# Performance work log

Measured on AMD Instinct MI355X. Metric: run time of the kernel, lower is better.

The kernel has to match this reference:

```python
import jax, jax.numpy as jnp
import numpy as np

TOPK = 2
NUM_EXPERTS = 8


def setup_inputs() -> dict:
    key = jax.random.key(0)
    k1, k2 = jax.random.split(key)
    T, H, E = 16384, 2048, NUM_EXPERTS
    x = jax.random.normal(k1, (T, H), dtype=jnp.float32)
    W = jax.random.normal(k2, (E, H), dtype=jnp.float32) * (1.0 / np.sqrt(H))
    return {"x": x, "W": W}


def reference(x, W):
    # gating: [T, H] @ [H, E] -> [T, E]
    logits = jnp.einsum("th,eh->te", x, W)
    # top-k expert selection (largest, sorted desc, matching torch.topk)
    top_logits, top_indices = jax.lax.top_k(logits, TOPK)
    # softmax over the k selected logits, computed in fp32 (torch: dtype=float32 then type_as)
    scores = jax.nn.softmax(top_logits.astype(jnp.float32), axis=-1).astype(logits.dtype)
    # histogram of expert assignments (torch.histc -> float counts)
    tokens_per_expert = jnp.bincount(top_indices.reshape(-1), length=NUM_EXPERTS).astype(jnp.float32)
    return scores, top_indices, tokens_per_expert
```

## Files before the change

kernel.cpp:

```cpp
#include <hip/hip_runtime.h>
#include <math.h>

#define HDIM 2048
#define NEXP 8
#define TB 4
#define BLOCK 256
#define WAVES_PB 4
#define TOK_PB (WAVES_PB * TB)
#define CH 256
#define NCH (HDIM / CH)

__global__ __launch_bounds__(BLOCK, 4) void
router_main(const float* __restrict__ x,
            const float* __restrict__ W,
            float* __restrict__ out_scores,
            float* __restrict__ out_idx,
            float* __restrict__ hist,
            int T)
{
    __shared__ float4 xs[2][WAVES_PB][TB][64];
    __shared__ int cnt[NEXP];
    if (threadIdx.x < NEXP) cnt[threadIdx.x] = 0;
    __syncthreads();

    const int lane = threadIdx.x & 63;
    const int wv   = threadIdx.x >> 6;
    const int tok0 = blockIdx.x * TOK_PB + wv * TB;

    const float* xsrc[TB];
#pragma unroll
    for (int t = 0; t < TB; ++t) {
        int tt = tok0 + t; if (tt > T - 1) tt = T - 1;
        xsrc[t] = x + (size_t)tt * HDIM + lane * 4;
    }
    const float* wb = W + lane * 4;

    float acc[TB * NEXP];
#pragma unroll
    for (int i = 0; i < TB * NEXP; ++i) acc[i] = 0.f;

#pragma unroll
    for (int t = 0; t < TB; ++t)
        __builtin_amdgcn_global_load_lds(
            (const __attribute__((address_space(1))) void*)(xsrc[t]),
            (__attribute__((address_space(3))) void*)&xs[0][wv][t][0],
            16, 0, 0);

#pragma unroll 1
    for (int c = 0; c < NCH; ++c) {
        const int h = c * CH;

        float4 w[NEXP];
#pragma unroll
        for (int e = 0; e < NEXP; ++e)
            w[e] = *reinterpret_cast<const float4*>(wb + (size_t)e * HDIM + h);

        asm volatile("" ::: "memory");

        if (c + 1 < NCH) {
#pragma unroll
            for (int t = 0; t < TB; ++t)
                __builtin_amdgcn_global_load_lds(
                    (const __attribute__((address_space(1))) void*)(xsrc[t] + h + CH),
                    (__attribute__((address_space(3))) void*)&xs[(c + 1) & 1][wv][t][0],
                    16, 0, 0);
        }

        asm volatile("s_waitcnt vmcnt(8)" ::: "memory");

#pragma unroll
        for (int t = 0; t < TB; ++t) {
            const float4 xv = xs[c & 1][wv][t][lane];
#pragma unroll
            for (int e = 0; e < NEXP; ++e) {
                float a = acc[t * NEXP + e];
                a = fmaf(xv.x, w[e].x, a);
                a = fmaf(xv.y, w[e].y, a);
                a = fmaf(xv.z, w[e].z, a);
                a = fmaf(xv.w, w[e].w, a);
                acc[t * NEXP + e] = a;
            }
        }
    }

#pragma unroll
    for (int j = 0; j < 32; ++j) acc[j] += __shfl_xor(acc[j], 32, 64);

#define FOLD(SM)                                                          \
    {                                                                     \
        const bool up = (lane & SM) != 0;                                 \
        _Pragma("unroll")                                                 \
        for (int j = 0; j < SM; ++j) {                                    \
            float keep = up ? acc[j + SM] : acc[j];                       \
            float send = up ? acc[j] : acc[j + SM];                       \
            acc[j] = keep + __shfl_xor(send, SM, 64);                     \
        }                                                                 \
    }
    FOLD(16) FOLD(8) FOLD(4) FOLD(2) FOLD(1)
#undef FOLD

    const int e_my  = lane & 7;
    const int t_loc = (lane & 31) >> 3;
    const float mylg = acc[0];

    float v1 = mylg;
    int   i1 = e_my;
#pragma unroll
    for (int m = 1; m <= 4; m <<= 1) {
        float ov = __shfl_xor(v1, m, 64);
        int   oi = __shfl_xor(i1, m, 64);
        if (ov > v1 || (ov == v1 && oi < i1)) { v1 = ov; i1 = oi; }
    }
    float v2 = (e_my == i1) ? -3.402823466e+38f : mylg;
    int   i2 = e_my;
#pragma unroll
    for (int m = 1; m <= 4; m <<= 1) {
        float ov = __shfl_xor(v2, m, 64);
        int   oi = __shfl_xor(i2, m, 64);
        if (ov > v2 || (ov == v2 && oi < i2)) { v2 = ov; i2 = oi; }
    }

    const float ed  = expf(v2 - v1);
    const float inv = 1.0f / (1.0f + ed);

    const int tok = tok0 + t_loc;
    if (lane < 32 && e_my == 0 && tok < T) {
        *reinterpret_cast<float2*>(out_scores + 2 * tok) = make_float2(inv, ed * inv);
        *reinterpret_cast<float2*>(out_idx    + 2 * tok) = make_float2((float)i1, (float)i2);
        atomicAdd(&cnt[i1], 1);
        atomicAdd(&cnt[i2], 1);
    }

    __syncthreads();
    if (threadIdx.x < NEXP)
        atomicAdd(&hist[threadIdx.x], (float)cnt[threadIdx.x]);
}

extern "C" void kernel_launch(void* const* d_in, const int* in_sizes, int n_in,
                              void* d_out, int out_size, void* d_ws, size_t ws_size,
                              hipStream_t stream)
{
    const float* x = (const float*)d_in[0];
    const float* W = (const float*)d_in[1];
    const int T = in_sizes[0] / HDIM;

    float* out        = (float*)d_out;
    float* out_scores = out;
    float* out_idx    = out + (size_t)2 * T;
    float* hist       = out + (size_t)4 * T;

    hipMemsetAsync(hist, 0, NEXP * sizeof(float), stream);

    const int nblocks = (T + TOK_PB - 1) / TOK_PB;
    router_main<<<nblocks, BLOCK, 0, stream>>>(x, W, out_scores, out_idx, hist, T);
}
```

Measured before the change: 39.96 us.

## Stage full gate weights in LDS, load x directly into registers

Result: slower. 42.37 us (+6.0%).

```diff
diff --git a/kernel.cpp b/kernel.cpp
--- a/kernel.cpp
+++ b/kernel.cpp
@@ -4,8 +4,8 @@
 #define HDIM 2048
 #define NEXP 8
 #define TB 4
-#define BLOCK 256
-#define WAVES_PB 4
+#define BLOCK 512
+#define WAVES_PB 8
 #define TOK_PB (WAVES_PB * TB)
 #define CH 256
 #define NCH (HDIM / CH)
@@ -18,8 +18,16 @@
             float* __restrict__ hist,
             int T)
 {
-    __shared__ float4 xs[2][WAVES_PB][TB][64];
+    __shared__ float wlds[NEXP][HDIM];
     __shared__ int cnt[NEXP];
+
+    {
+        const float4* __restrict__ Wv = reinterpret_cast<const float4*>(W);
+        float4* wl = reinterpret_cast<float4*>(&wlds[0][0]);
+#pragma unroll
+        for (int j = 0; j < (NEXP * HDIM / 4) / BLOCK; ++j)
+            wl[threadIdx.x + j * BLOCK] = Wv[threadIdx.x + j * BLOCK];
+    }
     if (threadIdx.x < NEXP) cnt[threadIdx.x] = 0;
     __syncthreads();
 
@@ -27,58 +35,50 @@
     const int wv   = threadIdx.x >> 6;
     const int tok0 = blockIdx.x * TOK_PB + wv * TB;
 
-    const float* xsrc[TB];
+    const float* xb[TB];
 #pragma unroll
     for (int t = 0; t < TB; ++t) {
         int tt = tok0 + t; if (tt > T - 1) tt = T - 1;
-        xsrc[t] = x + (size_t)tt * HDIM + lane * 4;
+        xb[t] = x + (size_t)tt * HDIM + lane * 4;
     }
-    const float* wb = W + lane * 4;
 
     float acc[TB * NEXP];
 #pragma unroll
     for (int i = 0; i < TB * NEXP; ++i) acc[i] = 0.f;
 
 #pragma unroll
-    for (int t = 0; t < TB; ++t)
-        __builtin_amdgcn_global_load_lds(
-            (const __attribute__((address_space(1))) void*)(xsrc[t]),
-            (__attribute__((address_space(3))) void*)&xs[0][wv][t][0],
-            16, 0, 0);
-
-#pragma unroll 1
     for (int c = 0; c < NCH; ++c) {
-        const int h = c * CH;
-
-        float4 w[NEXP];
+        const int h = c * CH + lane * 4;
+        float4 xv[TB];
 #pragma unroll
-        for (int e = 0; e < NEXP; ++e)
-            w[e] = *reinterpret_cast<const float4*>(wb + (size_t)e * HDIM + h);
-
-        asm volatile("" ::: "memory");
-
-        if (c + 1 < NCH) {
-#pragma unroll
-            for (int t = 0; t < TB; ++t)
-                __builtin_amdgcn_global_load_lds(
-                    (const __attribute__((address_space(1))) void*)(xsrc[t] + h + CH),
-                    (__attribute__((address_space(3))) void*)&xs[(c + 1) & 1][wv][t][0],
-                    16, 0, 0);
-        }
-
-        asm volatile("s_waitcnt vmcnt(8)" ::: "memory");
+        for (int t = 0; t < TB; ++t)
+            xv[t] = *reinterpret_cast<const float4*>(xb[t] + c * CH);
 
 #pragma unroll
-        for (int t = 0; t < TB; ++t) {
-            const float4 xv = xs[c & 1][wv][t][lane];
+        for (int half = 0; half < 2; ++half) {
+            const int b = half * 4;
+            float4 w0 = *reinterpret_cast<const float4*>(&wlds[b + 0][h]);
+            float4 w1 = *reinterpret_cast<const float4*>(&wlds[b + 1][h]);
+            float4 w2 = *reinterpret_cast<const float4*>(&wlds[b + 2][h]);
+            float4 w3 = *reinterpret_cast<const float4*>(&wlds[b + 3][h]);
 #pragma unroll
-            for (int e = 0; e < NEXP; ++e) {
-                float a = acc[t * NEXP + e];
-                a = fmaf(xv.x, w[e].x, a);
-                a = fmaf(xv.y, w[e].y, a);
-                a = fmaf(xv.z, w[e].z, a);
-                a = fmaf(xv.w, w[e].w, a);
-                acc[t * NEXP + e] = a;
+            for (int t = 0; t < TB; ++t) {
+                float a0 = acc[t * NEXP + b + 0];
+                float a1 = acc[t * NEXP + b + 1];
+                float a2 = acc[t * NEXP + b + 2];
+                float a3 = acc[t * NEXP + b + 3];
+                a0 = fmaf(xv[t].x, w0.x, a0); a0 = fmaf(xv[t].y, w0.y, a0);
+                a0 = fmaf(xv[t].z, w0.z, a0); a0 = fmaf(xv[t].w, w0.w, a0);
+                a1 = fmaf(xv[t].x, w1.x, a1); a1 = fmaf(xv[t].y, w1.y, a1);
+                a1 = fmaf(xv[t].z, w1.z, a1); a1 = fmaf(xv[t].w, w1.w, a1);
+                a2 = fmaf(xv[t].x, w2.x, a2); a2 = fmaf(xv[t].y, w2.y, a2);
+                a2 = fmaf(xv[t].z, w2.z, a2); a2 = fmaf(xv[t].w, w2.w, a2);
+                a3 = fmaf(xv[t].x, w3.x, a3); a3 = fmaf(xv[t].y, w3.y, a3);
+                a3 = fmaf(xv[t].z, w3.z, a3); a3 = fmaf(xv[t].w, w3.w, a3);
+                acc[t * NEXP + b + 0] = a0;
+                acc[t * NEXP + b + 1] = a1;
+                acc[t * NEXP + b + 2] = a2;
+                acc[t * NEXP + b + 3] = a3;
             }
         }
     }
```
